# Optimization experiments

Measured on AMD Instinct MI355X. Metric: run time of the kernel, lower is better.

Reference implementation:

```python
import jax, jax.numpy as jnp
import numpy as np

D_MODEL = 512
N_HEADS = 8
D_FF = 2048
WINDOW = 32
EPS = 1e-5


def _layernorm(x, g, b):
    mu = jnp.mean(x, axis=-1, keepdims=True)
    var = jnp.mean(jnp.square(x - mu), axis=-1, keepdims=True)
    return (x - mu) * jax.lax.rsqrt(var + EPS) * g + b


def setup_inputs() -> dict:
    key = jax.random.key(0)
    ks = jax.random.split(key, 12)
    B, S, D = 8, 8192, D_MODEL
    s = 0.02
    return {
        "x": jax.random.normal(ks[0], (B, S, D), dtype=jnp.float32),
        "Wq": jax.random.normal(ks[1], (D, D), dtype=jnp.float32) * s,
        "bq": jnp.zeros((D,), jnp.float32),
        "Wk": jax.random.normal(ks[2], (D, D), dtype=jnp.float32) * s,
        "bk": jnp.zeros((D,), jnp.float32),
        "Wv": jax.random.normal(ks[3], (D, D), dtype=jnp.float32) * s,
        "bv": jnp.zeros((D,), jnp.float32),
        "Wo": jax.random.normal(ks[4], (D, D), dtype=jnp.float32) * s,
        "bo": jnp.zeros((D,), jnp.float32),
        "g1": jnp.ones((D,), jnp.float32),
        "be1": jnp.zeros((D,), jnp.float32),
        "W1": jax.random.normal(ks[5], (D, D_FF), dtype=jnp.float32) * s,
        "b1": jnp.zeros((D_FF,), jnp.float32),
        "W2": jax.random.normal(ks[6], (D_FF, D), dtype=jnp.float32) * s,
        "b2": jnp.zeros((D,), jnp.float32),
        "g2": jnp.ones((D,), jnp.float32),
        "be2": jnp.zeros((D,), jnp.float32),
    }


def reference(x, Wq, bq, Wk, bk, Wv, bv, Wo, bo, g1, be1, W1, b1, W2, b2, g2, be2):
    B, S, D = x.shape
    H, W = N_HEADS, WINDOW
    dh = D // H
    nW = S // W

    def split(t):  # [B,S,D] -> [B,nW,W,H,dh]
        return t.reshape(B, nW, W, H, dh)

    q = split(x @ Wq + bq)
    k = split(x @ Wk + bk)
    v = split(x @ Wv + bv)

    # block-local (non-overlapping window) attention: [B,H,nW,W,W]
    scores = jnp.einsum('bnqhd,bnkhd->bhnqk', q, k) / jnp.sqrt(jnp.float32(dh))
    attn = jax.nn.softmax(scores, axis=-1)
    o = jnp.einsum('bhnqk,bnkhd->bnqhd', attn, v).reshape(B, S, D)
    attn_out = o @ Wo + bo

    x = _layernorm(x + attn_out, g1, be1)
    ff = jax.nn.relu(x @ W1 + b1) @ W2 + b2
    x = _layernorm(x + ff, g2, be2)
    return x
```

## Files before the change

kernel.cpp:

```cpp
#include <hip/hip_runtime.h>

typedef unsigned int uint;
typedef unsigned short ushort;

typedef __bf16 bf16x8 __attribute__((ext_vector_type(8)));
typedef float f32x4 __attribute__((ext_vector_type(4)));

#define AS1 __attribute__((address_space(1)))
#define AS3 __attribute__((address_space(3)))

__device__ __forceinline__ float bflo(uint u) { return __uint_as_float(u << 16); }
__device__ __forceinline__ float bfhi(uint u) { return __uint_as_float(u & 0xffff0000u); }
__device__ __forceinline__ ushort f2bf(float f) {
  uint u = __float_as_uint(f);
  u += 0x7fffu + ((u >> 16) & 1u);
  return (ushort)(u >> 16);
}
__device__ __forceinline__ uint pack2(float lo, float hi) {
  return (uint)f2bf(lo) | ((uint)f2bf(hi) << 16);
}

__global__ __launch_bounds__(256) void cvt_f32_bf16(
    const float* __restrict__ in, ushort* __restrict__ out)
{
  const long i = ((long)blockIdx.x * 256 + threadIdx.x) * 8;
  float4 a = *(const float4*)(in + i);
  float4 b = *(const float4*)(in + i + 4);
  uint4 r;
  r.x = pack2(a.x, a.y); r.y = pack2(a.z, a.w);
  r.z = pack2(b.x, b.y); r.w = pack2(b.z, b.w);
  *(uint4*)(out + i) = r;
}

__global__ __launch_bounds__(256) void transpose_wf(
    const float* __restrict__ in, ushort* __restrict__ out, int R, int Ccols)
{
  __shared__ float tile[32][33];
  const int tx = threadIdx.x, ty = threadIdx.y;
  const int c0 = blockIdx.x * 32, r0 = blockIdx.y * 32;
#pragma unroll
  for (int j = 0; j < 32; j += 8)
    tile[ty + j][tx] = in[(long)(r0 + ty + j) * Ccols + (c0 + tx)];
  __syncthreads();
#pragma unroll
  for (int j = 0; j < 32; j += 8)
    out[(long)(c0 + ty + j) * R + (r0 + tx)] = f2bf(tile[tx][ty + j]);
}

__global__ __launch_bounds__(512, 2) void gemm256(
    const ushort* __restrict__ A, const ushort* __restrict__ Bt,
    const float* __restrict__ bias, void* __restrict__ Cv,
    int M, int N, int K, int relu, int out_f32)
{
  __shared__ ushort lds[65536];
  const int t = threadIdx.x;
  const int w = t >> 6, l = t & 63;
  const int quad = l >> 4, l16 = l & 15;
  const int wm = w >> 2, wn = w & 3;

  const int gx = gridDim.x;
  int bid = blockIdx.y * gx + blockIdx.x;
  const int nwg = gx * gridDim.y;
  if ((nwg & 7) == 0) bid = (bid & 7) * (nwg >> 3) + (bid >> 3);
  const long m0 = (long)(bid / gx) * 256;
  const long n0 = (long)(bid % gx) * 256;

  const int lr = l >> 3;
  const int lc = l & 7;
  const int swc = lc ^ lr;
  int arow[2][2], brow[2][2];
#pragma unroll
  for (int s = 0; s < 2; ++s) {
    const int o = w * 2 + s;
    arow[0][s] = (o >> 3) * 128 + (o & 7) * 8;
    arow[1][s] = arow[0][s] + 64;
    brow[0][s] = (o >> 2) * 64 + (o & 3) * 8;
    brow[1][s] = brow[0][s] + 32;
  }
  uint aoff[2][2], boff[2][2];
#pragma unroll
  for (int X = 0; X < 2; ++X)
#pragma unroll
    for (int s = 0; s < 2; ++s) {
      aoff[X][s] = (uint)((m0 + arow[X][s] + lr) * (long)K + swc * 8);
      boff[X][s] = (uint)((n0 + brow[X][s] + lr) * (long)K + swc * 8);
    }

#define STAGE_A(X, kt) do { \
    __builtin_amdgcn_global_load_lds((const AS1 uint*)(A + aoff[X][0] + (uint)(kt) * 64u), \
        (AS3 uint*)(lds + (((kt) & 1) << 14) + arow[X][0] * 64), 16, 0, 0); \
    __builtin_amdgcn_global_load_lds((const AS1 uint*)(A + aoff[X][1] + (uint)(kt) * 64u), \
        (AS3 uint*)(lds + (((kt) & 1) << 14) + arow[X][1] * 64), 16, 0, 0); } while (0)
#define STAGE_B(Y, kt) do { \
    __builtin_amdgcn_global_load_lds((const AS1 uint*)(Bt + boff[Y][0] + (uint)(kt) * 64u), \
        (AS3 uint*)(lds + 32768 + (((kt) & 1) << 14) + brow[Y][0] * 64), 16, 0, 0); \
    __builtin_amdgcn_global_load_lds((const AS1 uint*)(Bt + boff[Y][1] + (uint)(kt) * 64u), \
        (AS3 uint*)(lds + 32768 + (((kt) & 1) << 14) + brow[Y][1] * 64), 16, 0, 0); } while (0)

  const int rswz0 = ((0 + quad) ^ (l16 & 7)) * 8;
  const int rswz1 = ((4 + quad) ^ (l16 & 7)) * 8;
  const int abase = wm * 8192 + l16 * 64;
  const int bbase = 32768 + wn * 4096 + l16 * 64;

  bf16x8 af[4][2], b0v[2][2], b1v[2][2];

#define LDA(mh, p) do { \
  _Pragma("unroll") for (int i_ = 0; i_ < 4; ++i_) { \
    af[i_][0] = *(const bf16x8*)(lds + ((p) << 14) + abase + ((mh) * 4 + i_) * 1024 + rswz0); \
    af[i_][1] = *(const bf16x8*)(lds + ((p) << 14) + abase + ((mh) * 4 + i_) * 1024 + rswz1); } } while (0)
#define LDB(nh, p, bq) do { \
  _Pragma("unroll") for (int j_ = 0; j_ < 2; ++j_) { \
    bq[j_][0] = *(const bf16x8*)(lds + ((p) << 14) + bbase + ((nh) * 2 + j_) * 1024 + rswz0); \
    bq[j_][1] = *(const bf16x8*)(lds + ((p) << 14) + bbase + ((nh) * 2 + j_) * 1024 + rswz1); } } while (0)
#define MFMAQ(mh, nh, bq) do { \
  __builtin_amdgcn_s_setprio(1); \
  _Pragma("unroll") for (int ks_ = 0; ks_ < 2; ++ks_) \
  _Pragma("unroll") for (int i_ = 0; i_ < 4; ++i_) \
  _Pragma("unroll") for (int j_ = 0; j_ < 2; ++j_) \
    acc[(mh) * 4 + i_][(nh) * 2 + j_] = __builtin_amdgcn_mfma_f32_16x16x32_bf16( \
        af[i_][ks_], bq[j_][ks_], acc[(mh) * 4 + i_][(nh) * 2 + j_], 0, 0, 0); \
  __builtin_amdgcn_s_setprio(0); } while (0)
#define BAR() __builtin_amdgcn_s_barrier()
#define WAITLGKM() asm volatile("s_waitcnt lgkmcnt(0)" ::: "memory")
#define WAITVM(n) asm volatile("s_waitcnt vmcnt(" #n ")" ::: "memory")

  f32x4 acc[8][4];
#pragma unroll
  for (int i = 0; i < 8; ++i)
#pragma unroll
    for (int j = 0; j < 4; ++j)
      acc[i][j] = f32x4{0.f, 0.f, 0.f, 0.f};

  const int NT = K >> 6;
  const int NIT = NT >> 1;

  STAGE_A(0, 0); STAGE_B(1, 0); STAGE_A(1, 0); STAGE_B(0, 0);
  STAGE_A(0, 1); STAGE_B(1, 1);
  WAITVM(4);
  BAR();

  for (int it = 0; it < NIT; ++it) {
    const int t1 = 2 * it + 1, t2 = 2 * it + 2, t3 = 2 * it + 3;
    const bool more = (t2 < NT);
    LDA(0, 0); LDB(0, 0, b0v);
    STAGE_A(1, t1);
    BAR(); WAITLGKM();
    MFMAQ(0, 0, b0v);
    BAR();
    LDB(1, 0, b1v);
    STAGE_B(0, t1);
    BAR(); WAITLGKM();
    MFMAQ(0, 1, b1v);
    BAR();
    LDA(1, 0);
    if (more) STAGE_A(0, t2);
    BAR(); WAITLGKM();
    MFMAQ(1, 1, b1v);
    BAR();
    LDB(0, 0, b0v);
    if (more) STAGE_B(1, t2);
    BAR(); WAITLGKM();
    MFMAQ(1, 0, b0v);
    if (more) { WAITVM(4); } else { WAITVM(0); }
    BAR();
    LDA(0, 1); LDB(0, 1, b0v);
    if (more) STAGE_A(1, t2);
    BAR(); WAITLGKM();
    MFMAQ(0, 0, b0v);
    BAR();
    LDB(1, 1, b1v);
    if (more) STAGE_B(0, t2);
    BAR(); WAITLGKM();
    MFMAQ(0, 1, b1v);
    BAR();
    LDA(1, 1);
    if (t3 < NT) STAGE_A(0, t3);
    BAR(); WAITLGKM();
    MFMAQ(1, 1, b1v);
    BAR();
    LDB(0, 1, b0v);
    if (t3 < NT) STAGE_B(1, t3);
    BAR(); WAITLGKM();
    MFMAQ(1, 0, b0v);
    if (more) { WAITVM(4); } else { WAITVM(0); }
    BAR();
  }

  if (!out_f32) {
    ushort* Cb = (ushort*)Cv;
#pragma unroll
    for (int hf = 0; hf < 2; ++hf) {
      if (wm == hf) {
#pragma unroll
        for (int in = 0; in < 4; ++in) {
          const int cl = wn * 64 + in * 16 + l16;
          const float bv = bias[n0 + cl];
#pragma unroll
          for (int im = 0; im < 8; ++im)
#pragma unroll
            for (int r = 0; r < 4; ++r) {
              float vv = acc[im][in][r] + bv;
              if (relu) vv = fmaxf(vv, 0.f);
              lds[(im * 16 + quad * 4 + r) * 264 + cl] = f2bf(vv);
            }
        }
      }
      __syncthreads();
#pragma unroll
      for (int it2 = 0; it2 < 8; ++it2) {
        const int idx = it2 * 512 + t;
        const int row = idx >> 5, c16 = idx & 31;
        uint4 d = *(const uint4*)(lds + row * 264 + c16 * 8);
        *(uint4*)(Cb + (m0 + hf * 128 + row) * (long)N + n0 + c16 * 8) = d;
      }
      __syncthreads();
    }
  } else {
    float* Cg = (float*)Cv;
    float* Cf = (float*)lds;
#pragma unroll
    for (int p = 0; p < 4; ++p) {
      if (wm == (p >> 1)) {
        const int imh = p & 1;
#pragma unroll
        for (int in = 0; in < 4; ++in) {
          const int cl = wn * 64 + in * 16 + l16;
          const float bv = bias[n0 + cl];
#pragma unroll
          for (int i = 0; i < 4; ++i)
#pragma unroll
            for (int r = 0; r < 4; ++r) {
              float vv = acc[imh * 4 + i][in][r] + bv;
              if (relu) vv = fmaxf(vv, 0.f);
              Cf[(i * 16 + quad * 4 + r) * 260 + cl] = vv;
            }
        }
      }
      __syncthreads();
#pragma unroll
      for (int it2 = 0; it2 < 8; ++it2) {
        const int idx = it2 * 512 + t;
        const int row = idx >> 6, c4 = idx & 63;
        float4 d = *(const float4*)(Cf + row * 260 + c4 * 4);
        *(float4*)(Cg + (m0 + p * 64 + row) * (long)N + n0 + c4 * 4) = d;
      }
      __syncthreads();
    }
  }
#undef STAGE_A
#undef STAGE_B
#undef LDA
#undef LDB
#undef MFMAQ
#undef BAR
#undef WAITLGKM
#undef WAITVM
}

__global__ __launch_bounds__(256, 2) void attn_mfma(
    ushort* qo, const ushort* __restrict__ k, const ushort* __restrict__ v)
{
  __shared__ ushort kv[32 * 512];
  __shared__ ushort pbuf[8][32 * 72];
  const int t = threadIdx.x;
  const int w = t >> 6, l = t & 63;
  const int quad = l >> 4, l16 = l & 15;
  const long base = (long)blockIdx.x * (32 * 512);

#pragma unroll
  for (int i = 0; i < 8; ++i) {
    const int c = w * 8 + i;
    __builtin_amdgcn_global_load_lds(
        (const AS1 uint*)(k + base + c * 512 + l * 8),
        (AS3 uint*)(kv + c * 512), 16, 0, 0);
  }
  bf16x8 qf[2][2][2];
#pragma unroll
  for (int hh = 0; hh < 2; ++hh) {
    const int h = w * 2 + hh;
#pragma unroll
    for (int mt = 0; mt < 2; ++mt)
#pragma unroll
      for (int ks = 0; ks < 2; ++ks)
        qf[hh][mt][ks] = *(const bf16x8*)(qo + base + (mt * 16 + l16) * 512 + h * 64 + ks * 32 + quad * 8);
  }
  __syncthreads();

#pragma unroll
  for (int hh = 0; hh < 2; ++hh) {
    const int h = w * 2 + hh;
    f32x4 sc[2][2];
#pragma unroll
    for (int mt = 0; mt < 2; ++mt)
#pragma unroll
      for (int nt = 0; nt < 2; ++nt)
        sc[mt][nt] = f32x4{0.f, 0.f, 0.f, 0.f};
#pragma unroll
    for (int ks = 0; ks < 2; ++ks) {
      bf16x8 kb0 = *(const bf16x8*)(kv + (0 * 16 + l16) * 512 + h * 64 + ks * 32 + quad * 8);
      bf16x8 kb1 = *(const bf16x8*)(kv + (1 * 16 + l16) * 512 + h * 64 + ks * 32 + quad * 8);
      sc[0][0] = __builtin_amdgcn_mfma_f32_16x16x32_bf16(qf[hh][0][ks], kb0, sc[0][0], 0, 0, 0);
      sc[0][1] = __builtin_amdgcn_mfma_f32_16x16x32_bf16(qf[hh][0][ks], kb1, sc[0][1], 0, 0, 0);
      sc[1][0] = __builtin_amdgcn_mfma_f32_16x16x32_bf16(qf[hh][1][ks], kb0, sc[1][0], 0, 0, 0);
      sc[1][1] = __builtin_amdgcn_mfma_f32_16x16x32_bf16(qf[hh][1][ks], kb1, sc[1][1], 0, 0, 0);
    }
    ushort* pb = pbuf[w * 2 + hh];
#pragma unroll
    for (int mt = 0; mt < 2; ++mt) {
#pragma unroll
      for (int r = 0; r < 4; ++r) {
        float a = sc[mt][0][r] * 0.125f;
        float b = sc[mt][1][r] * 0.125f;
        float mx = fmaxf(a, b);
        mx = fmaxf(mx, __shfl_xor(mx, 1));
        mx = fmaxf(mx, __shfl_xor(mx, 2));
        mx = fmaxf(mx, __shfl_xor(mx, 4));
        mx = fmaxf(mx, __shfl_xor(mx, 8));
        float ea = __expf(a - mx), eb = __expf(b - mx);
        float s = ea + eb;
        s += __shfl_xor(s, 1);
        s += __shfl_xor(s, 2);
        s += __shfl_xor(s, 4);
        s += __shfl_xor(s, 8);
        const float inv = 1.f / s;
        const int row = mt * 16 + quad * 4 + r;
        pb[row * 72 + 0 * 16 + l16] = f2bf(ea * inv);
        pb[row * 72 + 1 * 16 + l16] = f2bf(eb * inv);
      }
    }
  }
  __syncthreads();

#pragma unroll
  for (int i = 0; i < 8; ++i) {
    const int c = w * 8 + i;
    __builtin_amdgcn_global_load_lds(
        (const AS1 uint*)(v + base + c * 512 + l * 8),
        (AS3 uint*)(kv + c * 512), 16, 0, 0);
  }
  bf16x8 pf[2][2];
#pragma unroll
  for (int hh = 0; hh < 2; ++hh)
#pragma unroll
    for (int mt = 0; mt < 2; ++mt)
      pf[hh][mt] = *(const bf16x8*)(pbuf[w * 2 + hh] + (mt * 16 + l16) * 72 + quad * 8);
  __syncthreads();

#pragma unroll
  for (int hh = 0; hh < 2; ++hh) {
    const int h = w * 2 + hh;
    f32x4 oc[2][4];
#pragma unroll
    for (int mt = 0; mt < 2; ++mt)
#pragma unroll
      for (int nt = 0; nt < 4; ++nt)
        oc[mt][nt] = f32x4{0.f, 0.f, 0.f, 0.f};
#pragma unroll
    for (int nt = 0; nt < 4; ++nt) {
      bf16x8 bv;
#pragma unroll
      for (int j = 0; j < 8; ++j)
        bv[j] = ((const __bf16*)kv)[(quad * 8 + j) * 512 + h * 64 + nt * 16 + l16];
      oc[0][nt] = __builtin_amdgcn_mfma_f32_16x16x32_bf16(pf[hh][0], bv, oc[0][nt], 0, 0, 0);
      oc[1][nt] = __builtin_amdgcn_mfma_f32_16x16x32_bf16(pf[hh][1], bv, oc[1][nt], 0, 0, 0);
    }
    ushort* pb = pbuf[w * 2 + hh];
#pragma unroll
    for (int mt = 0; mt < 2; ++mt)
#pragma unroll
      for (int nt = 0; nt < 4; ++nt)
#pragma unroll
        for (int r = 0; r < 4; ++r)
          pb[(mt * 16 + quad * 4 + r) * 72 + nt * 16 + l16] = f2bf(oc[mt][nt][r]);
  }

#pragma unroll
  for (int i = 0; i < 8; ++i) {
    const int idx = i * 64 + l;
    const int hh = idx >> 8;
    const int row = (idx >> 3) & 31;
    const int c8 = idx & 7;
    uint4 d = *(const uint4*)(pbuf[w * 2 + hh] + row * 72 + c8 * 8);
    *(uint4*)(qo + base + row * 512 + (w * 2 + hh) * 64 + c8 * 8) = d;
  }
}

__global__ __launch_bounds__(256, 4) void ln1_res(
    const ushort* __restrict__ a, const ushort* __restrict__ b,
    const float* __restrict__ g, const float* __restrict__ be,
    ushort* __restrict__ out)
{
  const long row = (long)blockIdx.x * 4 + (threadIdx.x >> 6);
  const int lane = threadIdx.x & 63;
  const long off = row * 512 + lane * 8;
  uint4 ua = *(const uint4*)(a + off);
  uint4 ub = *(const uint4*)(b + off);
  float x[8];
  x[0] = bflo(ua.x) + bflo(ub.x); x[1] = bfhi(ua.x) + bfhi(ub.x);
  x[2] = bflo(ua.y) + bflo(ub.y); x[3] = bfhi(ua.y) + bfhi(ub.y);
  x[4] = bflo(ua.z) + bflo(ub.z); x[5] = bfhi(ua.z) + bfhi(ub.z);
  x[6] = bflo(ua.w) + bflo(ub.w); x[7] = bfhi(ua.w) + bfhi(ub.w);
  float sum = 0.f;
#pragma unroll
  for (int i = 0; i < 8; ++i) sum += x[i];
#pragma unroll
  for (int i = 1; i < 64; i <<= 1) sum += __shfl_xor(sum, i, 64);
  const float mu = sum * (1.0f / 512.0f);
  float vsum = 0.f;
#pragma unroll
  for (int i = 0; i < 8; ++i) { const float d = x[i] - mu; vsum += d * d; }
#pragma unroll
  for (int i = 1; i < 64; i <<= 1) vsum += __shfl_xor(vsum, i, 64);
  const float rs = rsqrtf(vsum * (1.0f / 512.0f) + 1e-5f);
  float4 g0 = *(const float4*)(g + lane * 8);
  float4 g1v = *(const float4*)(g + lane * 8 + 4);
  float4 e0 = *(const float4*)(be + lane * 8);
  float4 e1 = *(const float4*)(be + lane * 8 + 4);
  uint4 r;
  r.x = pack2((x[0] - mu) * rs * g0.x + e0.x, (x[1] - mu) * rs * g0.y + e0.y);
  r.y = pack2((x[2] - mu) * rs * g0.z + e0.z, (x[3] - mu) * rs * g0.w + e0.w);
  r.z = pack2((x[4] - mu) * rs * g1v.x + e1.x, (x[5] - mu) * rs * g1v.y + e1.y);
  r.w = pack2((x[6] - mu) * rs * g1v.z + e1.z, (x[7] - mu) * rs * g1v.w + e1.w);
  *(uint4*)(out + off) = r;
}

__global__ __launch_bounds__(256, 4) void ln2_res(
    const ushort* __restrict__ a, const float* bff,
    const float* __restrict__ g, const float* __restrict__ be,
    float* out)
{
  const long row = (long)blockIdx.x * 4 + (threadIdx.x >> 6);
  const int lane = threadIdx.x & 63;
  const long off = row * 512 + lane * 8;
  uint4 ua = *(const uint4*)(a + off);
  float4 fa = *(const float4*)(bff + off);
  float4 fb = *(const float4*)(bff + off + 4);
  float x[8];
  x[0] = bflo(ua.x) + fa.x; x[1] = bfhi(ua.x) + fa.y;
  x[2] = bflo(ua.y) + fa.z; x[3] = bfhi(ua.y) + fa.w;
  x[4] = bflo(ua.z) + fb.x; x[5] = bfhi(ua.z) + fb.y;
  x[6] = bflo(ua.w) + fb.z; x[7] = bfhi(ua.w) + fb.w;
  float sum = 0.f;
#pragma unroll
  for (int i = 0; i < 8; ++i) sum += x[i];
#pragma unroll
  for (int i = 1; i < 64; i <<= 1) sum += __shfl_xor(sum, i, 64);
  const float mu = sum * (1.0f / 512.0f);
  float vsum = 0.f;
#pragma unroll
  for (int i = 0; i < 8; ++i) { const float d = x[i] - mu; vsum += d * d; }
#pragma unroll
  for (int i = 1; i < 64; i <<= 1) vsum += __shfl_xor(vsum, i, 64);
  const float rs = rsqrtf(vsum * (1.0f / 512.0f) + 1e-5f);
  float4 g0 = *(const float4*)(g + lane * 8);
  float4 g1v = *(const float4*)(g + lane * 8 + 4);
  float4 e0 = *(const float4*)(be + lane * 8);
  float4 e1 = *(const float4*)(be + lane * 8 + 4);
  float4 r0, r1;
  r0.x = (x[0] - mu) * rs * g0.x + e0.x;
  r0.y = (x[1] - mu) * rs * g0.y + e0.y;
  r0.z = (x[2] - mu) * rs * g0.z + e0.z;
  r0.w = (x[3] - mu) * rs * g0.w + e0.w;
  r1.x = (x[4] - mu) * rs * g1v.x + e1.x;
  r1.y = (x[5] - mu) * rs * g1v.y + e1.y;
  r1.z = (x[6] - mu) * rs * g1v.z + e1.z;
  r1.w = (x[7] - mu) * rs * g1v.w + e1.w;
  *(float4*)(out + off) = r0;
  *(float4*)(out + off + 4) = r1;
}

extern "C" void kernel_launch(void* const* d_in, const int* in_sizes, int n_in,
                              void* d_out, int out_size, void* d_ws, size_t ws_size,
                              hipStream_t stream)
{
  const float* x   = (const float*)d_in[0];
  const float* Wq  = (const float*)d_in[1];
  const float* bq  = (const float*)d_in[2];
  const float* Wk  = (const float*)d_in[3];
  const float* bk  = (const float*)d_in[4];
  const float* Wv  = (const float*)d_in[5];
  const float* bv  = (const float*)d_in[6];
  const float* Wo  = (const float*)d_in[7];
  const float* bo  = (const float*)d_in[8];
  const float* g1  = (const float*)d_in[9];
  const float* be1 = (const float*)d_in[10];
  const float* W1  = (const float*)d_in[11];
  const float* b1  = (const float*)d_in[12];
  const float* W2  = (const float*)d_in[13];
  const float* b2  = (const float*)d_in[14];
  const float* g2  = (const float*)d_in[15];
  const float* be2 = (const float*)d_in[16];

  const long M = 65536;
  const size_t SZ = (size_t)M * 512;

  ushort* wsb = (ushort*)d_ws;
  ushort* xb  = wsb;
  ushort* R0  = wsb + SZ;
  ushort* Wqt = wsb + 2 * SZ;
  ushort* Wkt = Wqt + 512 * 512;
  ushort* Wvt = Wkt + 512 * 512;
  ushort* Wot = Wvt + 512 * 512;
  ushort* W1t = Wot + 512 * 512;
  ushort* W2t = W1t + 512 * 2048;

  ushort* outb = (ushort*)d_out;
  ushort* kb = outb;
  ushort* vb = outb + SZ;
  float* outf = (float*)d_out;

  dim3 tb(32, 8);
  transpose_wf<<<dim3(16, 16), tb, 0, stream>>>(Wq, Wqt, 512, 512);
  transpose_wf<<<dim3(16, 16), tb, 0, stream>>>(Wk, Wkt, 512, 512);
  transpose_wf<<<dim3(16, 16), tb, 0, stream>>>(Wv, Wvt, 512, 512);
  transpose_wf<<<dim3(16, 16), tb, 0, stream>>>(Wo, Wot, 512, 512);
  transpose_wf<<<dim3(64, 16), tb, 0, stream>>>(W1, W1t, 512, 2048);
  transpose_wf<<<dim3(16, 64), tb, 0, stream>>>(W2, W2t, 2048, 512);
  cvt_f32_bf16<<<dim3(16384), dim3(256), 0, stream>>>(x, xb);

  dim3 blk(512);
  gemm256<<<dim3(2, 256), blk, 0, stream>>>(xb, Wqt, bq, R0, 65536, 512, 512, 0, 0);
  gemm256<<<dim3(2, 256), blk, 0, stream>>>(xb, Wkt, bk, kb, 65536, 512, 512, 0, 0);
  gemm256<<<dim3(2, 256), blk, 0, stream>>>(xb, Wvt, bv, vb, 65536, 512, 512, 0, 0);
  attn_mfma<<<dim3(2048), dim3(256), 0, stream>>>(R0, kb, vb);
  gemm256<<<dim3(2, 256), blk, 0, stream>>>(R0, Wot, bo, outb, 65536, 512, 512, 0, 0);
  ln1_res<<<dim3(16384), dim3(256), 0, stream>>>(xb, outb, g1, be1, R0);
  for (int c = 0; c < 4; ++c) {
    const size_t rows0 = (size_t)c * 16384;
    gemm256<<<dim3(8, 64), blk, 0, stream>>>(R0 + rows0 * 512, W1t, b1, xb,
                                             16384, 2048, 512, 1, 0);
    gemm256<<<dim3(2, 64), blk, 0, stream>>>(xb, W2t, b2, outf + rows0 * 512,
                                             16384, 512, 2048, 0, 1);
  }
  ln2_res<<<dim3(16384), dim3(256), 0, stream>>>(R0, outf, g2, be2, outf);
}
```

Before: 1.046 ms.

## Fuse QKV projections into one GEMM launch; add 128x128 GEMM for FFN down-projection

The Q, K and V projections now run as a single gemm256 launch over a 1536-wide N dimension. Each block picks its bias and output pointer by which 512-column slice it covers. This relies on the three transposed weight matrices sitting contiguously in memory. Separately, the W2 down-projection (K=2048, N=512) switches to a new simpler 128x128-tile kernel, giving 512 blocks instead of 128 so more compute units are busy. That kernel has no software pipelining of its global-to-LDS loads, which could cost throughput per block.

```diff
diff --git a/kernel.cpp b/kernel.cpp
--- a/kernel.cpp
+++ b/kernel.cpp
@@ -49,8 +49,10 @@
 
 __global__ __launch_bounds__(512, 2) void gemm256(
     const ushort* __restrict__ A, const ushort* __restrict__ Bt,
-    const float* __restrict__ bias, void* __restrict__ Cv,
-    int M, int N, int K, int relu, int out_f32)
+    const float* __restrict__ bias0, const float* __restrict__ bias1,
+    const float* __restrict__ bias2,
+    void* __restrict__ Cv0, void* __restrict__ Cv1, void* __restrict__ Cv2,
+    int M, int N, int K, int relu, int out_f32, int split512)
 {
   __shared__ ushort lds[65536];
   const int t = threadIdx.x;
@@ -64,6 +66,16 @@
   if ((nwg & 7) == 0) bid = (bid & 7) * (nwg >> 3) + (bid >> 3);
   const long m0 = (long)(bid / gx) * 256;
   const long n0 = (long)(bid % gx) * 256;
+
+  long cn0 = n0;
+  const float* bsel = bias0;
+  void* Cvsel = Cv0;
+  if (split512) {
+    const int pi = (int)(n0 >> 9);
+    cn0 = n0 & 511;
+    if (pi == 1) { bsel = bias1; Cvsel = Cv1; }
+    else if (pi == 2) { bsel = bias2; Cvsel = Cv2; }
+  }
 
   const int lr = l >> 3;
   const int lc = l & 7;
@@ -187,14 +199,14 @@
   }
 
   if (!out_f32) {
-    ushort* Cb = (ushort*)Cv;
+    ushort* Cb = (ushort*)Cvsel;
 #pragma unroll
     for (int hf = 0; hf < 2; ++hf) {
       if (wm == hf) {
 #pragma unroll
         for (int in = 0; in < 4; ++in) {
           const int cl = wn * 64 + in * 16 + l16;
-          const float bv = bias[n0 + cl];
+          const float bv = bsel[cn0 + cl];
 #pragma unroll
           for (int im = 0; im < 8; ++im)
 #pragma unroll
@@ -211,12 +223,12 @@
         const int idx = it2 * 512 + t;
         const int row = idx >> 5, c16 = idx & 31;
         uint4 d = *(const uint4*)(lds + row * 264 + c16 * 8);
-        *(uint4*)(Cb + (m0 + hf * 128 + row) * (long)N + n0 + c16 * 8) = d;
+        *(uint4*)(Cb + (m0 + hf * 128 + row) * (long)N + cn0 + c16 * 8) = d;
       }
       __syncthreads();
     }
   } else {
-    float* Cg = (float*)Cv;
+    float* Cg = (float*)Cvsel;
     float* Cf = (float*)lds;
 #pragma unroll
     for (int p = 0; p < 4; ++p) {
@@ -225,7 +237,7 @@
 #pragma unroll
         for (int in = 0; in < 4; ++in) {
           const int cl = wn * 64 + in * 16 + l16;
-          const float bv = bias[n0 + cl];
+          const float bv = bsel[cn0 + cl];
 #pragma unroll
           for (int i = 0; i < 4; ++i)
 #pragma unroll
@@ -242,7 +254,7 @@
         const int idx = it2 * 512 + t;
         const int row = idx >> 6, c4 = idx & 63;
         float4 d = *(const float4*)(Cf + row * 260 + c4 * 4);
-        *(float4*)(Cg + (m0 + p * 64 + row) * (long)N + n0 + c4 * 4) = d;
+        *(float4*)(Cg + (m0 + p * 64 + row) * (long)N + cn0 + c4 * 4) = d;
       }
       __syncthreads();
     }
@@ -255,6 +267,134 @@
 #undef BAR
 #undef WAITLGKM
 #undef WAITVM
+}
+
+#define BM 128
+#define BN 128
+#define BKK 64
+#define CSTR 136
+#define FSTR 132
+
+__global__ __launch_bounds__(256, 2) void gemm_bt(
+    const ushort* __restrict__ A, const ushort* __restrict__ Bt,
+    const float* __restrict__ bias, void* __restrict__ Cv,
+    int M, int N, int K, int relu, int out_f32)
+{
+  __shared__ ushort smem[17408];
+  ushort* As = smem;
+  ushort* Bs = smem + BM * BKK;
+  const int t = threadIdx.x;
+  const int w = t >> 6, l = t & 63;
+  const int quad = l >> 4, l16 = l & 15;
+  const int wm = w & 1, wn = w >> 1;
+
+  const int gx = gridDim.x;
+  int bid = blockIdx.y * gx + blockIdx.x;
+  const int nwg = gx * gridDim.y;
+  if ((nwg & 7) == 0) bid = (bid & 7) * (nwg >> 3) + (bid >> 3);
+  const long m0 = (long)(bid / gx) * BM;
+  const long n0 = (long)(bid % gx) * BN;
+
+  const int srow = l >> 3;
+  const int scol = (l & 7) * 8;
+
+  f32x4 acc[4][4];
+#pragma unroll
+  for (int i = 0; i < 4; ++i)
+#pragma unroll
+    for (int j = 0; j < 4; ++j)
+      acc[i][j] = f32x4{0.f, 0.f, 0.f, 0.f};
+
+  for (int k0 = 0; k0 < K; k0 += BKK) {
+#pragma unroll
+    for (int i = 0; i < 4; ++i) {
+      const int chunk = w * 4 + i;
+      const int row = chunk * 8 + srow;
+      const ushort* ga = A + (m0 + row) * (long)K + k0 + scol;
+      const ushort* gb = Bt + (n0 + row) * (long)K + k0 + scol;
+      __builtin_amdgcn_global_load_lds(
+          (const AS1 uint*)ga, (AS3 uint*)(As + chunk * 512), 16, 0, 0);
+      __builtin_amdgcn_global_load_lds(
+          (const AS1 uint*)gb, (AS3 uint*)(Bs + chunk * 512), 16, 0, 0);
+    }
+    __syncthreads();
+#pragma unroll
+    for (int ks = 0; ks < 2; ++ks) {
+      bf16x8 af[4], bfr[4];
+#pragma unroll
+      for (int im = 0; im < 4; ++im)
+        af[im] = *(const bf16x8*)(As + (wm * 64 + im * 16 + l16) * BKK + ks * 32 + quad * 8);
+#pragma unroll
+      for (int in = 0; in < 4; ++in)
+        bfr[in] = *(const bf16x8*)(Bs + (wn * 64 + in * 16 + l16) * BKK + ks * 32 + quad * 8);
+#pragma unroll
+      for (int im = 0; im < 4; ++im)
+#pragma unroll
+        for (int in = 0; in < 4; ++in)
+          acc[im][in] = __builtin_amdgcn_mfma_f32_16x16x32_bf16(af[im], bfr[in], acc[im][in], 0, 0, 0);
+    }
+    __syncthreads();
+  }
+
+  if (!out_f32) {
+    ushort* Ct = smem;
+#pragma unroll
+    for (int in = 0; in < 4; ++in) {
+      const int cl = wn * 64 + in * 16 + l16;
+      const float bv = bias[n0 + cl];
+#pragma unroll
+      for (int im = 0; im < 4; ++im) {
+        const int rl = wm * 64 + im * 16 + quad * 4;
+#pragma unroll
+        for (int r = 0; r < 4; ++r) {
+          float vv = acc[im][in][r] + bv;
+          if (relu) vv = fmaxf(vv, 0.f);
+          Ct[(rl + r) * CSTR + cl] = f2bf(vv);
+        }
+      }
+    }
+    __syncthreads();
+    ushort* Cb = (ushort*)Cv;
+#pragma unroll
+    for (int it = 0; it < 8; ++it) {
+      const int idx = it * 256 + t;
+      const int row = idx >> 4, c16 = idx & 15;
+      uint4 d = *(const uint4*)(Ct + row * CSTR + c16 * 8);
+      *(uint4*)(Cb + (m0 + row) * (long)N + n0 + c16 * 8) = d;
+    }
+  } else {
+    float* Cf4 = (float*)smem;
+    float* Cg = (float*)Cv;
+#pragma unroll
+    for (int half = 0; half < 2; ++half) {
+      if (wm == half) {
+#pragma unroll
+        for (int in = 0; in < 4; ++in) {
+          const int cl = wn * 64 + in * 16 + l16;
+          const float bv = bias[n0 + cl];
+#pragma unroll
+          for (int im = 0; im < 4; ++im) {
+            const int rl = im * 16 + quad * 4;
+#pragma unroll
+            for (int r = 0; r < 4; ++r) {
+              float vv = acc[im][in][r] + bv;
+              if (relu) vv = fmaxf(vv, 0.f);
+              Cf4[(rl + r) * FSTR + cl] = vv;
+            }
+          }
+        }
+      }
+      __syncthreads();
+#pragma unroll
+      for (int it = 0; it < 8; ++it) {
+        const int idx = it * 256 + t;
+        const int row = idx >> 5, c4 = idx & 31;
+        float4 d = *(const float4*)(Cf4 + row * FSTR + c4 * 4);
+        *(float4*)(Cg + (m0 + half * 64 + row) * (long)N + n0 + c4 * 4) = d;
+      }
+      __syncthreads();
+    }
+  }
 }
 
 __global__ __launch_bounds__(256, 2) void attn_mfma(
@@ -519,18 +659,18 @@
   cvt_f32_bf16<<<dim3(16384), dim3(256), 0, stream>>>(x, xb);
 
   dim3 blk(512);
-  gemm256<<<dim3(2, 256), blk, 0, stream>>>(xb, Wqt, bq, R0, 65536, 512, 512, 0, 0);
-  gemm256<<<dim3(2, 256), blk, 0, stream>>>(xb, Wkt, bk, kb, 65536, 512, 512, 0, 0);
-  gemm256<<<dim3(2, 256), blk, 0, stream>>>(xb, Wvt, bv, vb, 65536, 512, 512, 0, 0);
+  gemm256<<<dim3(6, 256), blk, 0, stream>>>(xb, Wqt, bq, bk, bv,
+                                            R0, kb, vb, 65536, 512, 512, 0, 0, 1);
   attn_mfma<<<dim3(2048), dim3(256), 0, stream>>>(R0, kb, vb);
-  gemm256<<<dim3(2, 256), blk, 0, stream>>>(R0, Wot, bo, outb, 65536, 512, 512, 0, 0);
+  gemm256<<<dim3(2, 256), blk, 0, stream>>>(R0, Wot, bo, bo, bo,
+                                            outb, outb, outb, 65536, 512, 512, 0, 0, 0);
   ln1_res<<<dim3(16384), dim3(256), 0, stream>>>(xb, outb, g1, be1, R0);
   for (int c = 0; c < 4; ++c) {
     const size_t rows0 = (size_t)c * 16384;
-    gemm256<<<dim3(8, 64), blk, 0, stream>>>(R0 + rows0 * 512, W1t, b1, xb,
-                                             16384, 2048, 512, 1, 0);
-    gemm256<<<dim3(2, 64), blk, 0, stream>>>(xb, W2t, b2, outf + rows0 * 512,
-                                             16384, 512, 2048, 0, 1);
+    gemm256<<<dim3(8, 64), blk, 0, stream>>>(R0 + rows0 * 512, W1t, b1, b1, b1,
+                                             xb, xb, xb, 16384, 2048, 512, 1, 0, 0);
+    gemm_bt<<<dim3(4, 128), dim3(256), 0, stream>>>(xb, W2t, b2, outf + rows0 * 512,
+                                                    16384, 512, 2048, 0, 1);
   }
   ln2_res<<<dim3(16384), dim3(256), 0, stream>>>(R0, outf, g2, be2, outf);
 }
```

Result: faster. 991.8 us (-5.2%).
